# Kernel optimization log

Hardware: AMD Instinct MI355X
Metric: run time of the kernel (lower is better)

## Reference

```python
import jax, jax.numpy as jnp
import numpy as np

N_NODES = 150000
N_EDGES = 2400000
F_IN, HID, N_CLS = 22, 32, 6
BN_EPS = 1e-5


def setup_inputs() -> dict:
    key = jax.random.key(0)
    ks = jax.random.split(key, 10)
    x = jax.random.normal(ks[0], (N_NODES, F_IN), dtype=jnp.float32)
    edge_index = jax.random.randint(ks[1], (2, N_EDGES), 0, N_NODES, dtype=jnp.int64)
    # xavier-uniform style linear weights, zero biases (as in _init_weights)
    def xavier(k, fan_in, fan_out):
        lim = float(np.sqrt(6.0 / (fan_in + fan_out)))
        return jax.random.uniform(k, (fan_in, fan_out), jnp.float32, -lim, lim)
    return {
        "x": x,
        "edge_index": edge_index,
        "W_emb": xavier(ks[2], F_IN, HID),
        "b_emb": jnp.zeros((HID,), jnp.float32),
        "W_gcn": xavier(ks[3], HID, HID),
        "b_gcn": jnp.zeros((HID,), jnp.float32),
        "gamma": jnp.ones((HID,), jnp.float32),
        "beta": jnp.zeros((HID,), jnp.float32),
        "W_cls": xavier(ks[4], HID, N_CLS),
        "b_cls": jnp.zeros((N_CLS,), jnp.float32),
    }


def reference(x, edge_index, W_emb, b_emb, W_gcn, b_gcn, gamma, beta, W_cls, b_cls):
    N = x.shape[0]
    # embedding + relu
    h = jax.nn.relu(x @ W_emb + b_emb)                      # [N, HID]
    # GCNConv: linear transform first
    h = h @ W_gcn                                           # [N, HID]
    # add self-loops
    loops = jnp.arange(N, dtype=edge_index.dtype)
    src = jnp.concatenate([edge_index[0], loops])           # [E+N]
    dst = jnp.concatenate([edge_index[1], loops])
    # symmetric normalization deg^{-1/2} A_hat deg^{-1/2}
    deg = jax.ops.segment_sum(jnp.ones_like(dst, dtype=h.dtype), dst, num_segments=N)
    dis = jnp.where(deg > 0, jax.lax.rsqrt(jnp.where(deg > 0, deg, 1.0)), 0.0)
    norm = dis[src] * dis[dst]                              # [E+N]
    msg = h[src] * norm[:, None]                            # gather + scale
    agg = jax.ops.segment_sum(msg, dst, num_segments=N) + b_gcn
    # BatchNorm1d (training-mode batch statistics, biased variance)
    mean = jnp.mean(agg, axis=0)
    var = jnp.mean((agg - mean) ** 2, axis=0)
    hn = (agg - mean) * jax.lax.rsqrt(var + BN_EPS) * gamma + beta
    hn = jax.nn.relu(hn)
    # dropout is identity in eval; classifier
    return hn @ W_cls + b_cls
```

## Files before the change

### kernel.cpp

```cpp
#include <hip/hip_runtime.h>

#define N_NODES 150000
#define N_EDGES 2400000
#define F_IN    22
#define HID     32
#define N_CLS   6
#define BN_EPS  1e-5f

#define BSHIFT  8
#define BMASK   255
#define NB      ((N_NODES + BMASK) >> BSHIFT)
#define NBLK_BIN 256
#define CHUNK   ((N_EDGES + NBLK_BIN - 1) / NBLK_BIN)
#define CHUNK_H 8192
#define NBLK_H  ((N_EDGES + CHUNK_H - 1) / CHUNK_H)
#define EMB_NPB 64
#define NBLK_EMB ((N_NODES + EMB_NPB - 1) / EMB_NPB)
#define NREP    8

__device__ __forceinline__ unsigned bf16rne(float f) {
    unsigned u = __float_as_uint(f);
    return (u + 0x7FFFu + ((u >> 16) & 1u)) >> 16;
}
__device__ __forceinline__ float bflo(unsigned p) { return __uint_as_float(p << 16); }
__device__ __forceinline__ float bfhi(unsigned p) { return __uint_as_float(p & 0xFFFF0000u); }

__global__ void hist_kernel(const int* __restrict__ dst,
                            int* __restrict__ bcnt) {
    __shared__ int hloc[NB];
    for (int t = threadIdx.x; t < NB; t += 256) hloc[t] = 0;
    __syncthreads();
    int base = blockIdx.x * CHUNK_H;
    int end = base + CHUNK_H; if (end > N_EDGES) end = N_EDGES;
    int i = base + threadIdx.x;
    int d = 0;
    if (i < end) d = dst[i];
    while (i < end) {
        int inext = i + 256;
        int dn = 0;
        if (inext < end) dn = dst[inext];
        atomicAdd(&hloc[d >> BSHIFT], 1);
        d = dn; i = inext;
    }
    __syncthreads();
    for (int t = threadIdx.x; t < NB; t += 256)
        if (hloc[t]) atomicAdd(&bcnt[t], hloc[t]);
}

__global__ void embed_kernel(const float* __restrict__ x,
                             const float* __restrict__ W_emb,
                             const float* __restrict__ b_emb,
                             const float* __restrict__ W_gcn,
                             unsigned* __restrict__ hb) {
    __shared__ float sWe[F_IN * HID];
    __shared__ float sbe[HID];
    __shared__ float sWg[HID * HID];
    __shared__ float sx[EMB_NPB * 23];
    __shared__ float sh1[EMB_NPB * 33];
    __shared__ unsigned sp[EMB_NPB * 17];
    for (int t = threadIdx.x; t < F_IN * HID; t += 256) sWe[t] = W_emb[t];
    if (threadIdx.x < HID) sbe[threadIdx.x] = b_emb[threadIdx.x];
    for (int t = threadIdx.x; t < HID * HID; t += 256) sWg[t] = W_gcn[t];

    int nbase = blockIdx.x * EMB_NPB;
    int nvalid = N_NODES - nbase; if (nvalid > EMB_NPB) nvalid = EMB_NPB;

    {
        const float* xg = x + (size_t)nbase * F_IN;
        int totalx = nvalid * F_IN;
        for (int L = threadIdx.x; L < totalx; L += 256)
            sx[(L / F_IN) * 23 + (L % F_IN)] = xg[L];
    }
    __syncthreads();

    int n = threadIdx.x >> 2;
    int q = threadIdx.x & 3;
    bool act = n < nvalid;

    if (act) {
#pragma unroll
        for (int j = 0; j < 8; ++j) {
            float acc = sbe[q * 8 + j];
#pragma unroll
            for (int f = 0; f < F_IN; ++f)
                acc = fmaf(sx[n * 23 + f], sWe[f * HID + q * 8 + j], acc);
            sh1[n * 33 + q * 8 + j] = fmaxf(acc, 0.0f);
        }
    }
    __syncthreads();

    if (act) {
        float o[8];
#pragma unroll
        for (int j = 0; j < 8; ++j) o[j] = 0.0f;
#pragma unroll
        for (int f = 0; f < HID; ++f) {
            float hv = sh1[n * 33 + f];
#pragma unroll
            for (int j = 0; j < 8; ++j)
                o[j] = fmaf(hv, sWg[f * HID + q * 8 + j], o[j]);
        }
#pragma unroll
        for (int jj = 0; jj < 4; ++jj)
            sp[n * 17 + q * 4 + jj] = bf16rne(o[2 * jj]) | (bf16rne(o[2 * jj + 1]) << 16);
    }
    __syncthreads();

    int total = nvalid * 16;
    size_t gbase = (size_t)nbase * 16;
    for (int L = threadIdx.x; L < total; L += 256)
        hb[gbase + L] = sp[(L >> 4) * 17 + (L & 15)];
}

__global__ void bucket_scan_kernel(const int* __restrict__ bcnt,
                                   int* __restrict__ boff,
                                   int* __restrict__ bcur,
                                   float* __restrict__ stats) {
    int t = threadIdx.x;
    if (t < 64 * NREP) stats[t] = 0.0f;
    __shared__ int s[1024];
    int v0 = (t < NB) ? bcnt[t] : 0;
    s[t] = v0;
    __syncthreads();
#pragma unroll
    for (int o = 1; o < 1024; o <<= 1) {
        int v = (t >= o) ? s[t - o] : 0;
        __syncthreads();
        s[t] += v;
        __syncthreads();
    }
    if (t < NB) {
        int e = s[t] - v0;
        boff[t] = e;
        bcur[t] = e;
    }
    if (t == NB - 1) boff[NB] = s[t];
}

__global__ void bin_edges_kernel(const int* __restrict__ src,
                                 const int* __restrict__ dst,
                                 int* __restrict__ bcur,
                                 unsigned int* __restrict__ binned) {
    __shared__ int hloc[NB];
    __shared__ int base[NB];
    __shared__ int lcur[NB];
    for (int t = threadIdx.x; t < NB; t += 512) hloc[t] = 0;
    __syncthreads();

    int cbase = blockIdx.x * CHUNK;
    int cend = cbase + CHUNK; if (cend > N_EDGES) cend = N_EDGES;

    {
        int i = cbase + threadIdx.x;
        int d = 0;
        if (i < cend) d = dst[i];
        while (i < cend) {
            int inext = i + 512;
            int dn = 0;
            if (inext < cend) dn = dst[inext];
            atomicAdd(&hloc[d >> BSHIFT], 1);
            d = dn; i = inext;
        }
    }
    __syncthreads();
    for (int t = threadIdx.x; t < NB; t += 512) {
        int c = hloc[t];
        base[t] = c ? atomicAdd(&bcur[t], c) : 0;
        lcur[t] = 0;
    }
    __syncthreads();
    {
        int i = cbase + threadIdx.x;
        int d = 0, s = 0;
        if (i < cend) { d = dst[i]; s = src[i]; }
        while (i < cend) {
            int inext = i + 512;
            int dn = 0, sn = 0;
            if (inext < cend) { dn = dst[inext]; sn = src[inext]; }
            int b = d >> BSHIFT;
            int r = atomicAdd(&lcur[b], 1);
            binned[base[b] + r] = ((unsigned)(d & BMASK) << 24) | (unsigned)s;
            d = dn; s = sn; i = inext;
        }
    }
}

__global__ void bucket_csr_kernel(const int* __restrict__ boff,
                                  const unsigned int* __restrict__ binned,
                                  int* __restrict__ sorted_src,
                                  int* __restrict__ off,
                                  float* __restrict__ dis,
                                  unsigned* __restrict__ hb) {
    __shared__ int s_cnt[256];
    __shared__ int s_scan[256];
    __shared__ int s_cur[256];
    __shared__ float dl[256];
    int b = blockIdx.x;
    int t = threadIdx.x;
    int s0 = boff[b], s1 = boff[b + 1];
    int nbase = b << BSHIFT;
    int nnode = N_NODES - nbase; if (nnode > 256) nnode = 256;

    s_cnt[t] = 0;
    __syncthreads();
    for (int k = s0 + t; k < s1; k += 256)
        atomicAdd(&s_cnt[binned[k] >> 24], 1);
    __syncthreads();

    int v = s_cnt[t];
    s_scan[t] = v;
    __syncthreads();
#pragma unroll
    for (int o = 1; o < 256; o <<= 1) {
        int u = (t >= o) ? s_scan[t - o] : 0;
        __syncthreads();
        s_scan[t] += u;
        __syncthreads();
    }
    int excl = s_scan[t] - v;
    s_cur[t] = excl;
    float d = rsqrtf(1.0f + (float)v);
    dl[t] = d;
    if (t < nnode) {
        off[nbase + t] = s0 + excl;
        dis[nbase + t] = d;
    }
    if (b == NB - 1 && t == 0) off[N_NODES] = N_EDGES;
    __syncthreads();

    for (int k = s0 + t; k < s1; k += 256) {
        unsigned p = binned[k];
        int n = (int)(p >> 24);
        int r = atomicAdd(&s_cur[n], 1);
        sorted_src[s0 + r] = (int)(p & 0xFFFFFFu);
    }

    uint2* hv = reinterpret_cast<uint2*>(hb) + (size_t)nbase * 8;
    for (int tt = t; tt < nnode * 8; tt += 256) {
        uint2 w = hv[tt];
        float dd = dl[tt >> 3];
        w.x = bf16rne(bflo(w.x) * dd) | (bf16rne(bfhi(w.x) * dd) << 16);
        w.y = bf16rne(bflo(w.y) * dd) | (bf16rne(bfhi(w.y) * dd) << 16);
        hv[tt] = w;
    }
}

__global__ void aggregate_kernel(const int* __restrict__ off,
                                 const int* __restrict__ sorted_src,
                                 const unsigned* __restrict__ hb,
                                 const float* __restrict__ dis,
                                 float* __restrict__ agg,
                                 float* __restrict__ stats) {
    int t = blockIdx.x * blockDim.x + threadIdx.x;
    int node = t >> 3;
    int c = t & 7;
    bool active = node < N_NODES;

    float4 ps = {0.f, 0.f, 0.f, 0.f};
    float4 pq = {0.f, 0.f, 0.f, 0.f};

    if (active) {
        const uint2* hrow = reinterpret_cast<const uint2*>(hb);
        float dn = dis[node];
        uint2 hp = hrow[(size_t)node * 8 + c];
        float4 a0, a1, a2, a3;
        a0.x = bflo(hp.x); a0.y = bfhi(hp.x);
        a0.z = bflo(hp.y); a0.w = bfhi(hp.y);
        a1 = a2 = a3 = make_float4(0.f, 0.f, 0.f, 0.f);

        int b0 = off[node], e0 = off[node + 1];
        int cnt8 = (e0 - b0) >> 3;
        int k = b0;
        int p0 = 0, p1 = 0, p2 = 0, p3 = 0, p4 = 0, p5 = 0, p6 = 0, p7 = 0;
        if (cnt8 > 0) {
            p0 = sorted_src[k];     p1 = sorted_src[k + 1];
            p2 = sorted_src[k + 2]; p3 = sorted_src[k + 3];
            p4 = sorted_src[k + 4]; p5 = sorted_src[k + 5];
            p6 = sorted_src[k + 6]; p7 = sorted_src[k + 7];
        }
        for (int it = 0; it < cnt8; ++it) {
            int kn = k + 8;
            int n0 = p0, n1 = p1, n2 = p2, n3 = p3;
            int n4 = p4, n5 = p5, n6 = p6, n7 = p7;
            if (it + 1 < cnt8) {
                n0 = sorted_src[kn];     n1 = sorted_src[kn + 1];
                n2 = sorted_src[kn + 2]; n3 = sorted_src[kn + 3];
                n4 = sorted_src[kn + 4]; n5 = sorted_src[kn + 5];
                n6 = sorted_src[kn + 6]; n7 = sorted_src[kn + 7];
            }
            uint2 v0 = hrow[(size_t)p0 * 8 + c];
            uint2 v1 = hrow[(size_t)p1 * 8 + c];
            uint2 v2 = hrow[(size_t)p2 * 8 + c];
            uint2 v3 = hrow[(size_t)p3 * 8 + c];
            uint2 v4 = hrow[(size_t)p4 * 8 + c];
            uint2 v5 = hrow[(size_t)p5 * 8 + c];
            uint2 v6 = hrow[(size_t)p6 * 8 + c];
            uint2 v7 = hrow[(size_t)p7 * 8 + c];
            a0.x += bflo(v0.x); a0.y += bfhi(v0.x); a0.z += bflo(v0.y); a0.w += bfhi(v0.y);
            a1.x += bflo(v1.x); a1.y += bfhi(v1.x); a1.z += bflo(v1.y); a1.w += bfhi(v1.y);
            a2.x += bflo(v2.x); a2.y += bfhi(v2.x); a2.z += bflo(v2.y); a2.w += bfhi(v2.y);
            a3.x += bflo(v3.x); a3.y += bfhi(v3.x); a3.z += bflo(v3.y); a3.w += bfhi(v3.y);
            a0.x += bflo(v4.x); a0.y += bfhi(v4.x); a0.z += bflo(v4.y); a0.w += bfhi(v4.y);
            a1.x += bflo(v5.x); a1.y += bfhi(v5.x); a1.z += bflo(v5.y); a1.w += bfhi(v5.y);
            a2.x += bflo(v6.x); a2.y += bfhi(v6.x); a2.z += bflo(v6.y); a2.w += bfhi(v6.y);
            a3.x += bflo(v7.x); a3.y += bfhi(v7.x); a3.z += bflo(v7.y); a3.w += bfhi(v7.y);
            p0 = n0; p1 = n1; p2 = n2; p3 = n3;
            p4 = n4; p5 = n5; p6 = n6; p7 = n7;
            k = kn;
        }
        for (; k < e0; ++k) {
            int s = sorted_src[k];
            uint2 v = hrow[(size_t)s * 8 + c];
            a0.x += bflo(v.x); a0.y += bfhi(v.x);
            a0.z += bflo(v.y); a0.w += bfhi(v.y);
        }
        float4 o;
        o.x = (a0.x + a1.x + a2.x + a3.x) * dn;
        o.y = (a0.y + a1.y + a2.y + a3.y) * dn;
        o.z = (a0.z + a1.z + a2.z + a3.z) * dn;
        o.w = (a0.w + a1.w + a2.w + a3.w) * dn;
        reinterpret_cast<float4*>(agg)[(size_t)node * 8 + c] = o;
        ps = o;
        pq.x = o.x * o.x; pq.y = o.y * o.y; pq.z = o.z * o.z; pq.w = o.w * o.w;
    }

    __shared__ float S[256 * 4];
    __shared__ float Q[256 * 4];
    S[threadIdx.x * 4 + 0] = ps.x; S[threadIdx.x * 4 + 1] = ps.y;
    S[threadIdx.x * 4 + 2] = ps.z; S[threadIdx.x * 4 + 3] = ps.w;
    Q[threadIdx.x * 4 + 0] = pq.x; Q[threadIdx.x * 4 + 1] = pq.y;
    Q[threadIdx.x * 4 + 2] = pq.z; Q[threadIdx.x * 4 + 3] = pq.w;
    __syncthreads();
    if (threadIdx.x < 32) {
        int cc = threadIdx.x >> 2, j = threadIdx.x & 3;
        float s = 0.0f, q = 0.0f;
#pragma unroll
        for (int w = 0; w < 32; ++w) {
            int tid = (w << 3) | cc;
            s += S[tid * 4 + j];
            q += Q[tid * 4 + j];
        }
        float* rep = stats + 64 * (blockIdx.x & (NREP - 1));
        atomicAdd(&rep[threadIdx.x], s);
        atomicAdd(&rep[32 + threadIdx.x], q);
    }
}

__global__ void cls_kernel(const float* __restrict__ agg,
                           const float* __restrict__ stats,
                           const float* __restrict__ gamma,
                           const float* __restrict__ beta,
                           const float* __restrict__ W_cls,
                           const float* __restrict__ b_cls,
                           float* __restrict__ out) {
    __shared__ float sA[HID];
    __shared__ float sB[HID];
    __shared__ float sW[HID * N_CLS];
    __shared__ float sb[N_CLS];
    if (threadIdx.x < HID) {
        float sum = 0.0f, sq = 0.0f;
#pragma unroll
        for (int r = 0; r < NREP; ++r) {
            sum += stats[r * 64 + threadIdx.x];
            sq  += stats[r * 64 + 32 + threadIdx.x];
        }
        const float invN = 1.0f / (float)N_NODES;
        float mean = sum * invN;
        float var = sq * invN - mean * mean;
        float inv = rsqrtf(var + BN_EPS);
        float A = gamma[threadIdx.x] * inv;
        sA[threadIdx.x] = A;
        sB[threadIdx.x] = beta[threadIdx.x] - mean * A;
    }
    for (int t = threadIdx.x; t < HID * N_CLS; t += blockDim.x) sW[t] = W_cls[t];
    if (threadIdx.x < N_CLS) sb[threadIdx.x] = b_cls[threadIdx.x];
    __syncthreads();

    int i = blockIdx.x * blockDim.x + threadIdx.x;
    if (i >= N_NODES) return;

    float acc[N_CLS];
#pragma unroll
    for (int c = 0; c < N_CLS; ++c) acc[c] = sb[c];
#pragma unroll
    for (int f = 0; f < HID; ++f) {
        float t = fmaxf(fmaf(agg[(size_t)i * HID + f], sA[f], sB[f]), 0.0f);
#pragma unroll
        for (int c = 0; c < N_CLS; ++c) acc[c] = fmaf(t, sW[f * N_CLS + c], acc[c]);
    }
#pragma unroll
    for (int c = 0; c < N_CLS; ++c) out[(size_t)i * N_CLS + c] = acc[c];
}

extern "C" void kernel_launch(void* const* d_in, const int* in_sizes, int n_in,
                              void* d_out, int out_size, void* d_ws, size_t ws_size,
                              hipStream_t stream) {
    const float* x     = (const float*)d_in[0];
    const int*   edge  = (const int*)d_in[1];
    const float* W_emb = (const float*)d_in[2];
    const float* b_emb = (const float*)d_in[3];
    const float* W_gcn = (const float*)d_in[4];
    const float* gamma = (const float*)d_in[6];
    const float* beta  = (const float*)d_in[7];
    const float* W_cls = (const float*)d_in[8];
    const float* b_cls = (const float*)d_in[9];
    float* out = (float*)d_out;

    unsigned*     hb         = (unsigned*)d_ws;
    float*        agg        = (float*)(hb + (size_t)N_NODES * HID / 2);
    float*        dis        = agg + (size_t)N_NODES * HID;
    int*          off        = (int*)(dis + N_NODES);
    int*          bcnt       = off + N_NODES + 1;
    int*          boff       = bcnt + NB;
    int*          bcur       = boff + NB + 1;
    unsigned int* binned     = (unsigned int*)(bcur + NB);
    int*          sorted_src = (int*)(binned + N_EDGES);
    float*        stats      = (float*)(sorted_src + N_EDGES);

    hipMemsetAsync(bcnt, 0, NB * sizeof(int), stream);

    const int* src = edge;
    const int* dst = edge + N_EDGES;

    hist_kernel<<<NBLK_H, 256, 0, stream>>>(dst, bcnt);
    embed_kernel<<<NBLK_EMB, 256, 0, stream>>>(x, W_emb, b_emb, W_gcn, hb);
    bucket_scan_kernel<<<1, 1024, 0, stream>>>(bcnt, boff, bcur, stats);
    bin_edges_kernel<<<NBLK_BIN, 512, 0, stream>>>(src, dst, bcur, binned);
    bucket_csr_kernel<<<NB, 256, 0, stream>>>(boff, binned, sorted_src, off, dis, hb);
    aggregate_kernel<<<(N_NODES * 8 + 255) / 256, 256, 0, stream>>>(off, sorted_src,
                                                                    hb, dis, agg, stats);
    cls_kernel<<<(N_NODES + 255) / 256, 256, 0, stream>>>(agg, stats, gamma, beta,
                                                          W_cls, b_cls, out);
}
```

Before: 154.0 us.

## Register-block embed kernel over four nodes per thread and resize histogram grid

The embedding kernel now handles 256 nodes per block, and each thread computes four nodes times eight outputs in registers. Each weight read from shared memory is therefore reused four times. The bf16 results are written directly to global memory as 16-byte vector stores, which removes the shared staging buffer and one barrier. Separately, the histogram kernel switches to a fixed count of 1024 blocks with a derived chunk size. Risks include higher register pressure, larger shared memory per block lowering occupancy, and stale sx rows for the partial last block being computed but not stored.

```diff
diff --git a/kernel.cpp b/kernel.cpp
--- a/kernel.cpp
+++ b/kernel.cpp
@@ -12,9 +12,9 @@
 #define NB      ((N_NODES + BMASK) >> BSHIFT)
 #define NBLK_BIN 256
 #define CHUNK   ((N_EDGES + NBLK_BIN - 1) / NBLK_BIN)
-#define CHUNK_H 8192
-#define NBLK_H  ((N_EDGES + CHUNK_H - 1) / CHUNK_H)
-#define EMB_NPB 64
+#define NBLK_H  1024
+#define CHUNK_H ((N_EDGES + NBLK_H - 1) / NBLK_H)
+#define EMB_NPB 256
 #define NBLK_EMB ((N_NODES + EMB_NPB - 1) / EMB_NPB)
 #define NREP    8
 
@@ -57,7 +57,6 @@
     __shared__ float sWg[HID * HID];
     __shared__ float sx[EMB_NPB * 23];
     __shared__ float sh1[EMB_NPB * 33];
-    __shared__ unsigned sp[EMB_NPB * 17];
     for (int t = threadIdx.x; t < F_IN * HID; t += 256) sWe[t] = W_emb[t];
     if (threadIdx.x < HID) sbe[threadIdx.x] = b_emb[threadIdx.x];
     for (int t = threadIdx.x; t < HID * HID; t += 256) sWg[t] = W_gcn[t];
@@ -73,43 +72,69 @@
     }
     __syncthreads();
 
-    int n = threadIdx.x >> 2;
+    int g = threadIdx.x >> 2;
     int q = threadIdx.x & 3;
-    bool act = n < nvalid;
-
-    if (act) {
+
+    float a[4][8];
+#pragma unroll
+    for (int m = 0; m < 4; ++m)
+#pragma unroll
+        for (int j = 0; j < 8; ++j) a[m][j] = sbe[q * 8 + j];
+#pragma unroll
+    for (int f = 0; f < F_IN; ++f) {
+        float x0 = sx[(g * 4 + 0) * 23 + f];
+        float x1 = sx[(g * 4 + 1) * 23 + f];
+        float x2 = sx[(g * 4 + 2) * 23 + f];
+        float x3 = sx[(g * 4 + 3) * 23 + f];
 #pragma unroll
         for (int j = 0; j < 8; ++j) {
-            float acc = sbe[q * 8 + j];
-#pragma unroll
-            for (int f = 0; f < F_IN; ++f)
-                acc = fmaf(sx[n * 23 + f], sWe[f * HID + q * 8 + j], acc);
-            sh1[n * 33 + q * 8 + j] = fmaxf(acc, 0.0f);
-        }
-    }
-    __syncthreads();
-
-    if (act) {
-        float o[8];
-#pragma unroll
-        for (int j = 0; j < 8; ++j) o[j] = 0.0f;
-#pragma unroll
-        for (int f = 0; f < HID; ++f) {
-            float hv = sh1[n * 33 + f];
-#pragma unroll
-            for (int j = 0; j < 8; ++j)
-                o[j] = fmaf(hv, sWg[f * HID + q * 8 + j], o[j]);
-        }
-#pragma unroll
-        for (int jj = 0; jj < 4; ++jj)
-            sp[n * 17 + q * 4 + jj] = bf16rne(o[2 * jj]) | (bf16rne(o[2 * jj + 1]) << 16);
-    }
-    __syncthreads();
-
-    int total = nvalid * 16;
-    size_t gbase = (size_t)nbase * 16;
-    for (int L = threadIdx.x; L < total; L += 256)
-        hb[gbase + L] = sp[(L >> 4) * 17 + (L & 15)];
+            float w = sWe[f * HID + q * 8 + j];
+            a[0][j] = fmaf(x0, w, a[0][j]);
+            a[1][j] = fmaf(x1, w, a[1][j]);
+            a[2][j] = fmaf(x2, w, a[2][j]);
+            a[3][j] = fmaf(x3, w, a[3][j]);
+        }
+    }
+#pragma unroll
+    for (int m = 0; m < 4; ++m)
+#pragma unroll
+        for (int j = 0; j < 8; ++j)
+            sh1[(g * 4 + m) * 33 + q * 8 + j] = fmaxf(a[m][j], 0.0f);
+    __syncthreads();
+
+    float o[4][8];
+#pragma unroll
+    for (int m = 0; m < 4; ++m)
+#pragma unroll
+        for (int j = 0; j < 8; ++j) o[m][j] = 0.0f;
+#pragma unroll
+    for (int f = 0; f < HID; ++f) {
+        float h0 = sh1[(g * 4 + 0) * 33 + f];
+        float h1 = sh1[(g * 4 + 1) * 33 + f];
+        float h2 = sh1[(g * 4 + 2) * 33 + f];
+        float h3 = sh1[(g * 4 + 3) * 33 + f];
+#pragma unroll
+        for (int j = 0; j < 8; ++j) {
+            float w = sWg[f * HID + q * 8 + j];
+            o[0][j] = fmaf(h0, w, o[0][j]);
+            o[1][j] = fmaf(h1, w, o[1][j]);
+            o[2][j] = fmaf(h2, w, o[2][j]);
+            o[3][j] = fmaf(h3, w, o[3][j]);
+        }
+    }
+    uint4* hb4 = reinterpret_cast<uint4*>(hb);
+#pragma unroll
+    for (int m = 0; m < 4; ++m) {
+        int n = g * 4 + m;
+        if (n < nvalid) {
+            uint4 u;
+            u.x = bf16rne(o[m][0]) | (bf16rne(o[m][1]) << 16);
+            u.y = bf16rne(o[m][2]) | (bf16rne(o[m][3]) << 16);
+            u.z = bf16rne(o[m][4]) | (bf16rne(o[m][5]) << 16);
+            u.w = bf16rne(o[m][6]) | (bf16rne(o[m][7]) << 16);
+            hb4[(size_t)(nbase + n) * 4 + q] = u;
+        }
+    }
 }
 
 __global__ void bucket_scan_kernel(const int* __restrict__ bcnt,
```

Measured after the change: 403.3 us. 2.62x slower.
